# Performance work log

Measured on AMD Instinct MI355X. Metric: run time of the kernel, lower is better.

The kernel has to match this reference:

```python
import jax, jax.numpy as jnp
import numpy as np

EPS = 1e-5
K_NN = 5

def _bn(x, g, b, m, v):
    # BatchNorm1d in eval mode (running stats)
    return (x - m) * g / jnp.sqrt(v + EPS) + b

def _transf(x, w1, b1, g1, be1, m1, v1, w2, b2, g2, be2, m2, v2):
    h = jax.nn.relu(_bn(x @ w1.T + b1, g1, be1, m1, v1))
    return jax.nn.relu(_bn(h @ w2.T + b2, g2, be2, m2, v2))

def _cdist(x, y):
    # euclidean pairwise distance [Nq, Nk]
    d2 = jnp.sum(x * x, 1)[:, None] + jnp.sum(y * y, 1)[None, :] - 2.0 * (x @ y.T)
    return jnp.sqrt(jnp.clip(d2, 0.0))

def _to_pix(f):
    # [B,C,H,W] -> [B*H*W, C]
    B, C, H, W = f.shape
    return f.transpose(1, 0, 2, 3).reshape(C, -1).T

def _to_fmap(p, shape):
    B, C, H, W = shape
    return p.T.reshape(C, B, H, W).transpose(1, 0, 2, 3)

def _attend(dq, dk, aq, ak, vals, c1w, c1b, c2w, c2b):
    # full pairwise distance + hard kNN mask + softplus/softmax attention
    d = _cdist(dq, dk)                                  # [Nq, Nk]
    kth = -jax.lax.top_k(-d, K_NN)[0][:, K_NN - 1]       # K-th smallest per row
    # Conv1d(kernel_size = feat_dim) over length-feat_dim signal == dot product + bias
    att = (aq @ c1w + c1b)[:, None] + (ak @ c2w + c2b)[None, :]
    att = jax.nn.softplus(att) + jnp.where(d > kth[:, None], -1e9, 0.0)
    att = jax.nn.softmax(att, axis=1)
    return att @ vals

def _forward(inp_cont, inp_style, peers_cont, peers_style,
             w1c, b1c, g1c, be1c, m1c, v1c, w2c, b2c, g2c, be2c, m2c, v2c,
             c1cw, c1cb, c2cw, c2cb,
             w1s, b1s, g1s, be1s, m1s, v1s, w2s, b2s, g2s, be2s, m2s, v2s,
             c1sw, c1sb, c2sw, c2sb):
    ip = _to_pix(inp_cont)      # [N, C]
    pp = _to_pix(peers_cont)    # [N, C]
    ps = _to_pix(peers_style)   # [N, 2C]
    # recompose style: distance in content space, gather peer style
    aq = _transf(ip, w1c, b1c, g1c, be1c, m1c, v1c, w2c, b2c, g2c, be2c, m2c, v2c)
    ak = _transf(pp, w1c, b1c, g1c, be1c, m1c, v1c, w2c, b2c, g2c, be2c, m2c, v2c)
    out_sty = _attend(ip, pp, aq, ak, ps, c1cw, c1cb, c2cw, c2cb)   # [N, 2C]
    # recompose content: distance in (recomposed) style space, gather peer content
    sq = _transf(out_sty, w1s, b1s, g1s, be1s, m1s, v1s, w2s, b2s, g2s, be2s, m2s, v2s)
    sk = _transf(ps, w1s, b1s, g1s, be1s, m1s, v1s, w2s, b2s, g2s, be2s, m2s, v2s)
    out_cont = _attend(out_sty, ps, sq, sk, pp, c1sw, c1sb, c2sw, c2sb)  # [N, C]
    out_cont_f = _to_fmap(out_cont, inp_cont.shape)
    out_sty_f = _to_fmap(out_sty, inp_style.shape)
    return jnp.concatenate([out_cont_f, out_sty_f], axis=1)

def setup_inputs() -> dict:
    ks = jax.random.split(jax.random.key(0), 64)
    it = iter(range(64))
    rn = lambda sh, s=0.05: jax.random.normal(ks[next(it)], sh, jnp.float32) * s
    un = lambda sh: jax.random.uniform(ks[next(it)], sh, jnp.float32, 0.5, 1.5)
    C = 256; B = 1; H = W = 64
    return dict(
        inp_cont=rn((B, C, H, W), 1.0), inp_style=rn((B, 2 * C, H, W), 1.0),
        peers_cont=rn((B, C, H, W), 1.0), peers_style=rn((B, 2 * C, H, W), 1.0),
        w1c=rn((C // 2, C)), b1c=rn((C // 2,)), g1c=un((C // 2,)), be1c=rn((C // 2,)), m1c=rn((C // 2,)), v1c=un((C // 2,)),
        w2c=rn((C // 4, C // 2)), b2c=rn((C // 4,)), g2c=un((C // 4,)), be2c=rn((C // 4,)), m2c=rn((C // 4,)), v2c=un((C // 4,)),
        c1cw=rn((C // 4,)), c1cb=rn(()), c2cw=rn((C // 4,)), c2cb=rn(()),
        w1s=rn((C, 2 * C)), b1s=rn((C,)), g1s=un((C,)), be1s=rn((C,)), m1s=rn((C,)), v1s=un((C,)),
        w2s=rn((C // 2, C)), b2s=rn((C // 2,)), g2s=un((C // 2,)), be2s=rn((C // 2,)), m2s=rn((C // 2,)), v2s=un((C // 2,)),
        c1sw=rn((C // 2,)), c1sb=rn(()), c2sw=rn((C // 2,)), c2sb=rn(()),
    )

def reference(inp_cont, inp_style, peers_cont, peers_style,
              w1c, b1c, g1c, be1c, m1c, v1c, w2c, b2c, g2c, be2c, m2c, v2c,
              c1cw, c1cb, c2cw, c2cb,
              w1s, b1s, g1s, be1s, m1s, v1s, w2s, b2s, g2s, be2s, m2s, v2s,
              c1sw, c1sb, c2sw, c2sb):
    return _forward(inp_cont, inp_style, peers_cont, peers_style,
                    w1c, b1c, g1c, be1c, m1c, v1c, w2c, b2c, g2c, be2c, m2c, v2c,
                    c1cw, c1cb, c2cw, c2cb,
                    w1s, b1s, g1s, be1s, m1s, v1s, w2s, b2s, g2s, be2s, m2s, v2s,
                    c1sw, c1sb, c2sw, c2sb)
```

## Files before the change

kernel.cpp:

```cpp
#include <hip/hip_runtime.h>
#include <math.h>

#pragma clang fp contract(off)

#define NPIX 4096
#define BIGF 3.0e38f
#define SLOTS 8


__device__ __forceinline__ void ins5v(float v, float dl[5]) {
    if (v >= dl[4]) return;
    dl[4] = v;
#pragma unroll
    for (int u = 4; u > 0; --u)
        if (dl[u] < dl[u - 1]) { float t_ = dl[u]; dl[u] = dl[u - 1]; dl[u - 1] = t_; }
}

__device__ __forceinline__ float softplus_np(float x) {
    if (x > 0.f) {
        float ef = (float)exp((double)(-x));
        return x + (float)log1p((double)ef);
    } else if (x < 0.f) {
        float ef = (float)exp((double)x);
        return (float)log1p((double)ef);
    }
    return 0.69314718055994530942f;
}


__global__ __launch_bounds__(256) void gemm_bn_relu2_kernel(
    const float* __restrict__ W,
    const float* __restrict__ Xa, const float* __restrict__ Xb,
    const float* __restrict__ b, const float* __restrict__ g,
    const float* __restrict__ be, const float* __restrict__ m,
    const float* __restrict__ v,
    float* __restrict__ Ha, float* __restrict__ Hb, int M, int K) {
    const float* X = blockIdx.z ? Xb : Xa;
    float* H = blockIdx.z ? Hb : Ha;
    __shared__ float Ws[16][68];
    __shared__ float Xs[16][68];
    int t = threadIdx.x;
    int tx = t & 15, ty = t >> 4;
    int n0 = blockIdx.x * 64, m0 = blockIdx.y * 64;
    int wm = t >> 2, wk = (t & 3) * 4;
    int xk = t >> 4, xn = (t & 15) * 4;
    float acc[4][4] = {};
    for (int k0 = 0; k0 < K; k0 += 16) {
        float4 wv = *(const float4*)&W[(size_t)(m0 + wm) * K + k0 + wk];
        Ws[wk + 0][wm] = wv.x; Ws[wk + 1][wm] = wv.y;
        Ws[wk + 2][wm] = wv.z; Ws[wk + 3][wm] = wv.w;
        *(float4*)&Xs[xk][xn] = *(const float4*)&X[(size_t)(k0 + xk) * NPIX + n0 + xn];
        __syncthreads();
#pragma unroll
        for (int kk = 0; kk < 16; ++kk) {
            float4 a4 = *(float4*)&Ws[kk][ty * 4];
            float4 b4 = *(float4*)&Xs[kk][tx * 4];
            float ar[4] = {a4.x, a4.y, a4.z, a4.w};
            float br[4] = {b4.x, b4.y, b4.z, b4.w};
#pragma unroll
            for (int i = 0; i < 4; ++i)
#pragma unroll
                for (int j = 0; j < 4; ++j)
                    acc[i][j] = fmaf(ar[i], br[j], acc[i][j]);
        }
        __syncthreads();
    }
#pragma unroll
    for (int i = 0; i < 4; ++i) {
        int mrow = m0 + ty * 4 + i;
        float bb = b[mrow];
        float mm_ = m[mrow];
        float gg = g[mrow];
        float vv = v[mrow] + 1e-5f;
        float ss = (float)sqrt((double)vv);
        float bee = be[mrow];
        float o[4];
#pragma unroll
        for (int j = 0; j < 4; ++j) {
            float t0 = acc[i][j] + bb;
            t0 = t0 - mm_;
            t0 = t0 * gg;
            t0 = (float)((double)t0 / (double)ss);
            t0 = t0 + bee;
            o[j] = fmaxf(t0, 0.f);
        }
        *(float4*)&H[(size_t)mrow * NPIX + n0 + tx * 4] = *(float4*)&o[0];
    }
}


__global__ void dotk_np2_kernel(const float* __restrict__ Ha, const float* __restrict__ Hb,
                                const float* __restrict__ cwa, const float* __restrict__ cba,
                                const float* __restrict__ cwb, const float* __restrict__ cbb,
                                float* __restrict__ outa, float* __restrict__ outb, int C) {
    const float* H = blockIdx.z ? Hb : Ha;
    const float* cw = blockIdx.z ? cwb : cwa;
    const float* cb = blockIdx.z ? cbb : cba;
    float* out = blockIdx.z ? outb : outa;
    int p = blockIdx.x * 256 + threadIdx.x;
    float s = 0.f;
#pragma unroll 8
    for (int c = 0; c < C; ++c) s = fmaf(H[(size_t)c * NPIX + p], cw[c], s);
    out[p] = s + cb[0];
}


__global__ void skn_np2_kernel(const float* __restrict__ Ya, const float* __restrict__ Yb,
                               float* __restrict__ skna, float* __restrict__ sknb, int C) {
    const float* Y = blockIdx.z ? Yb : Ya;
    float* skn = blockIdx.z ? sknb : skna;
    int nb = C >> 7;
    int ppb = 256 / nb;
    int t = threadIdx.x;
    int pl = t % ppb;
    int b = t / ppb;
    int p = blockIdx.x * ppb + pl;
    __shared__ float sh[256];

    int c0 = b << 7;
    float r[8];
#pragma unroll
    for (int k = 0; k < 8; ++k) {
        float y = Y[(size_t)(c0 + k) * NPIX + p];
        r[k] = y * y;
    }
    for (int i = 8; i < 128; i += 8) {
#pragma unroll
        for (int k = 0; k < 8; ++k) {
            float y = Y[(size_t)(c0 + i + k) * NPIX + p];
            float q = y * y;
            r[k] = r[k] + q;
        }
    }
    sh[b * ppb + pl] = ((r[0] + r[1]) + (r[2] + r[3])) + ((r[4] + r[5]) + (r[6] + r[7]));
    __syncthreads();
    if (b == 0) {
        float s;
        if (nb == 2) s = sh[pl] + sh[ppb + pl];
        else s = (sh[pl] + sh[ppb + pl]) + (sh[2 * ppb + pl] + sh[3 * ppb + pl]);
        skn[p] = s;
    }
}


__global__ __launch_bounds__(256) void dist_np_kernel(
    const float* __restrict__ XT, const float* __restrict__ YT,
    const float* __restrict__ sknq, const float* __restrict__ sknk,
    float* __restrict__ D, int C, int qbase) {
    __shared__ float Xs[2][16][68];
    __shared__ float Ys[2][16][16][12];
    int t = threadIdx.x;
    int tx = t & 15, ty = t >> 4;
    int q0 = qbase + blockIdx.y * 64;
    int k0 = blockIdx.x * 128;
    float acc[4][8] = {};
    float4 xr = *(const float4*)&XT[(size_t)ty * NPIX + q0 + tx * 4];
    float4 yr0 = *(const float4*)&YT[(size_t)ty * NPIX + k0 + tx * 8];
    float4 yr1 = *(const float4*)&YT[(size_t)ty * NPIX + k0 + tx * 8 + 4];
    *(float4*)&Xs[0][ty][tx * 4] = xr;
    *(float4*)&Ys[0][ty][tx][0] = yr0;
    *(float4*)&Ys[0][ty][tx][4] = yr1;
    __syncthreads();
    int nt = C >> 4;
    for (int tt2 = 0; tt2 < nt; ++tt2) {
        int cur = tt2 & 1;
        if (tt2 + 1 < nt) {
            int cn = (tt2 + 1) << 4;
            xr = *(const float4*)&XT[(size_t)(cn + ty) * NPIX + q0 + tx * 4];
            yr0 = *(const float4*)&YT[(size_t)(cn + ty) * NPIX + k0 + tx * 8];
            yr1 = *(const float4*)&YT[(size_t)(cn + ty) * NPIX + k0 + tx * 8 + 4];
        }
#pragma unroll
        for (int kk = 0; kk < 16; ++kk) {
            float4 a4 = *(float4*)&Xs[cur][kk][ty * 4];
            float4 b40 = *(float4*)&Ys[cur][kk][tx][0];
            float4 b41 = *(float4*)&Ys[cur][kk][tx][4];
            float ar[4] = {a4.x, a4.y, a4.z, a4.w};
            float br[8] = {b40.x, b40.y, b40.z, b40.w, b41.x, b41.y, b41.z, b41.w};
#pragma unroll
            for (int i = 0; i < 4; ++i)
#pragma unroll
                for (int j = 0; j < 8; ++j)
                    acc[i][j] = fmaf(ar[i], br[j], acc[i][j]);
        }
        if (tt2 + 1 < nt) {
            *(float4*)&Xs[cur ^ 1][ty][tx * 4] = xr;
            *(float4*)&Ys[cur ^ 1][ty][tx][0] = yr0;
            *(float4*)&Ys[cur ^ 1][ty][tx][4] = yr1;
        }
        __syncthreads();
    }
    float sk8[8];
    *(float4*)&sk8[0] = *(const float4*)&sknk[k0 + tx * 8];
    *(float4*)&sk8[4] = *(const float4*)&sknk[k0 + tx * 8 + 4];
#pragma unroll
    for (int i = 0; i < 4; ++i) {
        float sq = sknq[q0 + ty * 4 + i];
        int lq = q0 - qbase + ty * 4 + i;
        float tmp[8];
#pragma unroll
        for (int j = 0; j < 8; ++j) {
            float A = sq + sk8[j];
            float B = 2.0f * acc[i][j];
            float d2 = A - B;
            float dc = fmaxf(d2, 0.f);
            tmp[j] = (float)sqrt((double)dc);
        }
        *(float4*)&D[(size_t)lq * NPIX + k0 + tx * 8] = *(float4*)&tmp[0];
        *(float4*)&D[(size_t)lq * NPIX + k0 + tx * 8 + 4] = *(float4*)&tmp[4];
    }
}


__global__ __launch_bounds__(256) void row_select_np_kernel(
    const float* __restrict__ D, const float* __restrict__ qs, const float* __restrict__ ks,
    int* __restrict__ isel, float* __restrict__ wsel, int qbase) {
    int p = qbase + blockIdx.x;
    const float* drow = D + (size_t)blockIdx.x * NPIX;
    int t = threadIdx.x;
    __shared__ float tops[256][5];
    __shared__ float l2[64][5];
    __shared__ float l3[16][5];
    __shared__ float kth_sh;
    __shared__ int cnt;
    __shared__ int slotj[16];
    __shared__ int n_sh;
    __shared__ float as_[16];
    __shared__ float evs[16];
    __shared__ float mx_sh, ssum_sh;

    if (t == 0) cnt = 0;
    float vcache[16];
    *(float4*)&vcache[0] = *(const float4*)&drow[t * 16];
    *(float4*)&vcache[4] = *(const float4*)&drow[t * 16 + 4];
    *(float4*)&vcache[8] = *(const float4*)&drow[t * 16 + 8];
    *(float4*)&vcache[12] = *(const float4*)&drow[t * 16 + 12];
    float dl[5] = {BIGF, BIGF, BIGF, BIGF, BIGF};
#pragma unroll
    for (int u = 0; u < 16; ++u) ins5v(vcache[u], dl);
#pragma unroll
    for (int u = 0; u < 5; ++u) tops[t][u] = dl[u];
    __syncthreads();
    if (t < 64) {
        float md[5] = {BIGF, BIGF, BIGF, BIGF, BIGF};
        for (int i = 0; i < 4; ++i)
            for (int u = 0; u < 5; ++u) ins5v(tops[t * 4 + i][u], md);
#pragma unroll
        for (int u = 0; u < 5; ++u) l2[t][u] = md[u];
    }
    __syncthreads();
    if (t < 16) {
        float md[5] = {BIGF, BIGF, BIGF, BIGF, BIGF};
        for (int i = 0; i < 4; ++i)
            for (int u = 0; u < 5; ++u) ins5v(l2[t * 4 + i][u], md);
#pragma unroll
        for (int u = 0; u < 5; ++u) l3[t][u] = md[u];
    }
    __syncthreads();
    if (t == 0) {
        float md[5] = {BIGF, BIGF, BIGF, BIGF, BIGF};
        for (int i = 0; i < 16; ++i)
            for (int u = 0; u < 5; ++u) ins5v(l3[i][u], md);
        kth_sh = md[4];
    }
    __syncthreads();
    float kth = kth_sh;
#pragma unroll
    for (int u = 0; u < 16; ++u) {
        if (vcache[u] <= kth) {
            int s = atomicAdd(&cnt, 1);
            if (s < 16) slotj[s] = t * 16 + u;
        }
    }
    __syncthreads();
    if (t == 0) {
        int n = cnt < 16 ? cnt : 16;
        for (int a = 1; a < n; ++a) {
            int key = slotj[a]; int b = a - 1;
            while (b >= 0 && slotj[b] > key) { slotj[b + 1] = slotj[b]; --b; }
            slotj[b + 1] = key;
        }
        n_sh = n;
    }
    __syncthreads();
    int n = n_sh;
    if (t < n) {
        float x = qs[p] + ks[slotj[t]];
        as_[t] = softplus_np(x);
    }
    __syncthreads();
    if (t == 0) {
        float mx = -BIGF;
        for (int s = 0; s < n; ++s) mx = fmaxf(mx, as_[s]);
        mx_sh = mx;
    }
    __syncthreads();
    if (t < n) evs[t] = (float)exp((double)(as_[t] - mx_sh));
    __syncthreads();
    if (t == 0) {
        float bs[32];
        for (int i = 0; i < 32; ++i) bs[i] = 0.f;
        int s2 = 0;
        while (s2 < n) {
            int b = slotj[s2] >> 7;
            float r[8] = {0.f, 0.f, 0.f, 0.f, 0.f, 0.f, 0.f, 0.f};
            while (s2 < n && (slotj[s2] >> 7) == b) {
                int res = slotj[s2] & 7;
                r[res] = r[res] + evs[s2];
                ++s2;
            }
            bs[b] = ((r[0] + r[1]) + (r[2] + r[3])) + ((r[4] + r[5]) + (r[6] + r[7]));
        }
        float t16[16], t8[8], t4[4], t2[2];
        for (int i = 0; i < 16; ++i) t16[i] = bs[2 * i] + bs[2 * i + 1];
        for (int i = 0; i < 8; ++i) t8[i] = t16[2 * i] + t16[2 * i + 1];
        for (int i = 0; i < 4; ++i) t4[i] = t8[2 * i] + t8[2 * i + 1];
        for (int i = 0; i < 2; ++i) t2[i] = t4[2 * i] + t4[2 * i + 1];
        ssum_sh = t2[0] + t2[1];
    }
    __syncthreads();
    if (t < SLOTS) {
        float w = (t < n) ? (float)((double)evs[t] / (double)ssum_sh) : 0.f;
        wsel[t * NPIX + p] = w;
        isel[t * NPIX + p] = (t < n) ? slotj[t] : 0;
    }
}


__global__ void gather_np_kernel(const float* __restrict__ V,
                                 const int* __restrict__ isel, const float* __restrict__ wsel,
                                 float* __restrict__ out, int CV) {
    int g = blockIdx.x * 256 + threadIdx.x;
    int p = g & (NPIX - 1);
    int c = g >> 12;
    if (c >= CV) return;
    const float* Vc = V + (size_t)c * NPIX;
    float s = 0.f;
#pragma unroll
    for (int tt = 0; tt < SLOTS; ++tt) {
        float w = wsel[tt * NPIX + p];
        int j = isel[tt * NPIX + p];
        s = fmaf(w, Vc[j], s);
    }
    out[(size_t)c * NPIX + p] = s;
}


extern "C" void kernel_launch(void* const* d_in, const int* in_sizes, int n_in,
                              void* d_out, int out_size, void* d_ws, size_t ws_size,
                              hipStream_t stream) {
    const float* ip = (const float*)d_in[0];
    const float* pp = (const float*)d_in[2];
    const float* ps = (const float*)d_in[3];
    const float* w1c = (const float*)d_in[4];
    const float* b1c = (const float*)d_in[5];
    const float* g1c = (const float*)d_in[6];
    const float* be1c = (const float*)d_in[7];
    const float* m1c = (const float*)d_in[8];
    const float* v1c = (const float*)d_in[9];
    const float* w2c = (const float*)d_in[10];
    const float* b2c = (const float*)d_in[11];
    const float* g2c = (const float*)d_in[12];
    const float* be2c = (const float*)d_in[13];
    const float* m2c = (const float*)d_in[14];
    const float* v2c = (const float*)d_in[15];
    const float* c1cw = (const float*)d_in[16];
    const float* c1cb = (const float*)d_in[17];
    const float* c2cw = (const float*)d_in[18];
    const float* c2cb = (const float*)d_in[19];
    const float* w1s = (const float*)d_in[20];
    const float* b1s = (const float*)d_in[21];
    const float* g1s = (const float*)d_in[22];
    const float* be1s = (const float*)d_in[23];
    const float* m1s = (const float*)d_in[24];
    const float* v1s = (const float*)d_in[25];
    const float* w2s = (const float*)d_in[26];
    const float* b2s = (const float*)d_in[27];
    const float* g2s = (const float*)d_in[28];
    const float* be2s = (const float*)d_in[29];
    const float* m2s = (const float*)d_in[30];
    const float* v2s = (const float*)d_in[31];
    const float* c1sw = (const float*)d_in[32];
    const float* c1sb = (const float*)d_in[33];
    const float* c2sw = (const float*)d_in[34];
    const float* c2sb = (const float*)d_in[35];

    float* out_cont = (float*)d_out;
    float* out_sty = (float*)d_out + 256 * NPIX;

    float* ws = (float*)d_ws;
    float* QS   = ws + 0;
    float* KS   = ws + 4096;
    float* SKNQ = ws + 8192;
    float* SKNK = ws + 12288;
    float* WSEL = ws + 16384;
    int*   ISEL = (int*)(ws + 49152);
    float* H1A  = ws + 81920;
    float* H1B  = ws + 1130496;
    float* H2A  = ws + 2179072;
    float* H2B  = ws + 2703360;
    float* D    = ws + 3227648;

    size_t base = 3227648;
    int chunk = 256;
    if (ws_size >= (base + (size_t)4096 * NPIX) * 4) chunk = 4096;
    else if (ws_size >= (base + (size_t)2048 * NPIX) * 4) chunk = 2048;
    else if (ws_size >= (base + (size_t)1024 * NPIX) * 4) chunk = 1024;
    else if (ws_size >= (base + (size_t)512 * NPIX) * 4) chunk = 512;
    int nch = NPIX / chunk;

    gemm_bn_relu2_kernel<<<dim3(64, 2, 2), 256, 0, stream>>>(
        w1c, ip, pp, b1c, g1c, be1c, m1c, v1c, H1A, H1B, 128, 256);
    gemm_bn_relu2_kernel<<<dim3(64, 1, 2), 256, 0, stream>>>(
        w2c, H1A, H1B, b2c, g2c, be2c, m2c, v2c, H2A, H2B, 64, 128);
    dotk_np2_kernel<<<dim3(16, 1, 2), 256, 0, stream>>>(
        H2A, H2B, c1cw, c1cb, c2cw, c2cb, QS, KS, 64);
    skn_np2_kernel<<<dim3(32, 1, 2), 256, 0, stream>>>(ip, pp, SKNQ, SKNK, 256);
    for (int ch = 0; ch < nch; ++ch) {
        dist_np_kernel<<<dim3(32, chunk / 64), 256, 0, stream>>>(ip, pp, SKNQ, SKNK, D, 256, ch * chunk);
        row_select_np_kernel<<<chunk, 256, 0, stream>>>(D, QS, KS, ISEL, WSEL, ch * chunk);
    }
    gather_np_kernel<<<(512 * NPIX) / 256, 256, 0, stream>>>(ps, ISEL, WSEL, out_sty, 512);

    gemm_bn_relu2_kernel<<<dim3(64, 4, 2), 256, 0, stream>>>(
        w1s, out_sty, ps, b1s, g1s, be1s, m1s, v1s, H1A, H1B, 256, 512);
    gemm_bn_relu2_kernel<<<dim3(64, 2, 2), 256, 0, stream>>>(
        w2s, H1A, H1B, b2s, g2s, be2s, m2s, v2s, H2A, H2B, 128, 256);
    dotk_np2_kernel<<<dim3(16, 1, 2), 256, 0, stream>>>(
        H2A, H2B, c1sw, c1sb, c2sw, c2sb, QS, KS, 128);
    skn_np2_kernel<<<dim3(64, 1, 2), 256, 0, stream>>>(out_sty, ps, SKNQ, SKNK, 512);
    for (int ch = 0; ch < nch; ++ch) {
        dist_np_kernel<<<dim3(32, chunk / 64), 256, 0, stream>>>(out_sty, ps, SKNQ, SKNK, D, 512, ch * chunk);
        row_select_np_kernel<<<chunk, 256, 0, stream>>>(D, QS, KS, ISEL, WSEL, ch * chunk);
    }
    gather_np_kernel<<<(256 * NPIX) / 256, 256, 0, stream>>>(pp, ISEL, WSEL, out_cont, 256);
}
```

Before: 561.9 us.

## Merge dot-product and squared-norm kernels; single-buffer LDS in distance GEMM

The per-pixel attention dot-product and squared-norm kernels are merged into one launch that picks its task from blockIdx.y, removing one launch per stage. Separately, the distance GEMM goes from double-buffered to single-buffered shared-memory tiles with a register prefetch, halving LDS use per block, which may allow more blocks per CU. The cost is an extra barrier per tile, so shared-memory stores no longer overlap the FMA loop, plus some idle blocks in the merged launch that exit early.

```diff
diff --git a/kernel.cpp b/kernel.cpp
--- a/kernel.cpp
+++ b/kernel.cpp
@@ -89,56 +89,59 @@
 }
 
 
-__global__ void dotk_np2_kernel(const float* __restrict__ Ha, const float* __restrict__ Hb,
-                                const float* __restrict__ cwa, const float* __restrict__ cba,
-                                const float* __restrict__ cwb, const float* __restrict__ cbb,
-                                float* __restrict__ outa, float* __restrict__ outb, int C) {
-    const float* H = blockIdx.z ? Hb : Ha;
-    const float* cw = blockIdx.z ? cwb : cwa;
-    const float* cb = blockIdx.z ? cbb : cba;
-    float* out = blockIdx.z ? outb : outa;
-    int p = blockIdx.x * 256 + threadIdx.x;
-    float s = 0.f;
+__global__ void util_np_kernel(
+    const float* __restrict__ H2A, const float* __restrict__ H2B,
+    const float* __restrict__ cwa, const float* __restrict__ cba,
+    const float* __restrict__ cwb, const float* __restrict__ cbb,
+    float* __restrict__ QS, float* __restrict__ KS, int CH,
+    const float* __restrict__ Yq, const float* __restrict__ Yk,
+    float* __restrict__ SKNQ, float* __restrict__ SKNK, int CY) {
+    int task = blockIdx.y;
+    int t = threadIdx.x;
+    if (task < 2) {
+        if (blockIdx.x >= 16) return;
+        const float* H = task ? H2B : H2A;
+        const float* cw = task ? cwb : cwa;
+        const float* cb = task ? cbb : cba;
+        float* out = task ? KS : QS;
+        int p = blockIdx.x * 256 + t;
+        float s = 0.f;
 #pragma unroll 8
-    for (int c = 0; c < C; ++c) s = fmaf(H[(size_t)c * NPIX + p], cw[c], s);
-    out[p] = s + cb[0];
-}
-
-
-__global__ void skn_np2_kernel(const float* __restrict__ Ya, const float* __restrict__ Yb,
-                               float* __restrict__ skna, float* __restrict__ sknb, int C) {
-    const float* Y = blockIdx.z ? Yb : Ya;
-    float* skn = blockIdx.z ? sknb : skna;
-    int nb = C >> 7;
-    int ppb = 256 / nb;
-    int t = threadIdx.x;
-    int pl = t % ppb;
-    int b = t / ppb;
-    int p = blockIdx.x * ppb + pl;
-    __shared__ float sh[256];
-
-    int c0 = b << 7;
-    float r[8];
-#pragma unroll
-    for (int k = 0; k < 8; ++k) {
-        float y = Y[(size_t)(c0 + k) * NPIX + p];
-        r[k] = y * y;
-    }
-    for (int i = 8; i < 128; i += 8) {
+        for (int c = 0; c < CH; ++c) s = fmaf(H[(size_t)c * NPIX + p], cw[c], s);
+        out[p] = s + cb[0];
+    } else {
+        const float* Y = (task == 2) ? Yq : Yk;
+        float* skn = (task == 2) ? SKNQ : SKNK;
+        int nb = CY >> 7;
+        int ppb = 256 / nb;
+        if (blockIdx.x * ppb >= NPIX) return;
+        int pl = t % ppb;
+        int b = t / ppb;
+        int p = blockIdx.x * ppb + pl;
+        __shared__ float sh[256];
+        int c0 = b << 7;
+        float r[8];
 #pragma unroll
         for (int k = 0; k < 8; ++k) {
-            float y = Y[(size_t)(c0 + i + k) * NPIX + p];
-            float q = y * y;
-            r[k] = r[k] + q;
-        }
-    }
-    sh[b * ppb + pl] = ((r[0] + r[1]) + (r[2] + r[3])) + ((r[4] + r[5]) + (r[6] + r[7]));
-    __syncthreads();
-    if (b == 0) {
-        float s;
-        if (nb == 2) s = sh[pl] + sh[ppb + pl];
-        else s = (sh[pl] + sh[ppb + pl]) + (sh[2 * ppb + pl] + sh[3 * ppb + pl]);
-        skn[p] = s;
+            float y = Y[(size_t)(c0 + k) * NPIX + p];
+            r[k] = y * y;
+        }
+        for (int i = 8; i < 128; i += 8) {
+#pragma unroll
+            for (int k = 0; k < 8; ++k) {
+                float y = Y[(size_t)(c0 + i + k) * NPIX + p];
+                float q = y * y;
+                r[k] = r[k] + q;
+            }
+        }
+        sh[b * ppb + pl] = ((r[0] + r[1]) + (r[2] + r[3])) + ((r[4] + r[5]) + (r[6] + r[7]));
+        __syncthreads();
+        if (b == 0) {
+            float s;
+            if (nb == 2) s = sh[pl] + sh[ppb + pl];
+            else s = (sh[pl] + sh[ppb + pl]) + (sh[2 * ppb + pl] + sh[3 * ppb + pl]);
+            skn[p] = s;
+        }
     }
 }
 
@@ -147,8 +150,8 @@
     const float* __restrict__ XT, const float* __restrict__ YT,
     const float* __restrict__ sknq, const float* __restrict__ sknk,
     float* __restrict__ D, int C, int qbase) {
-    __shared__ float Xs[2][16][68];
-    __shared__ float Ys[2][16][16][12];
+    __shared__ float Xs[16][68];
+    __shared__ float Ys[16][16][12];
     int t = threadIdx.x;
     int tx = t & 15, ty = t >> 4;
     int q0 = qbase + blockIdx.y * 64;
@@ -157,24 +160,21 @@
     float4 xr = *(const float4*)&XT[(size_t)ty * NPIX + q0 + tx * 4];
     float4 yr0 = *(const float4*)&YT[(size_t)ty * NPIX + k0 + tx * 8];
     float4 yr1 = *(const float4*)&YT[(size_t)ty * NPIX + k0 + tx * 8 + 4];
-    *(float4*)&Xs[0][ty][tx * 4] = xr;
-    *(float4*)&Ys[0][ty][tx][0] = yr0;
-    *(float4*)&Ys[0][ty][tx][4] = yr1;
-    __syncthreads();
-    int nt = C >> 4;
-    for (int tt2 = 0; tt2 < nt; ++tt2) {
-        int cur = tt2 & 1;
-        if (tt2 + 1 < nt) {
-            int cn = (tt2 + 1) << 4;
-            xr = *(const float4*)&XT[(size_t)(cn + ty) * NPIX + q0 + tx * 4];
-            yr0 = *(const float4*)&YT[(size_t)(cn + ty) * NPIX + k0 + tx * 8];
-            yr1 = *(const float4*)&YT[(size_t)(cn + ty) * NPIX + k0 + tx * 8 + 4];
+    for (int c0 = 0; c0 < C; c0 += 16) {
+        *(float4*)&Xs[ty][tx * 4] = xr;
+        *(float4*)&Ys[ty][tx][0] = yr0;
+        *(float4*)&Ys[ty][tx][4] = yr1;
+        __syncthreads();
+        if (c0 + 16 < C) {
+            xr = *(const float4*)&XT[(size_t)(c0 + 16 + ty) * NPIX + q0 + tx * 4];
+            yr0 = *(const float4*)&YT[(size_t)(c0 + 16 + ty) * NPIX + k0 + tx * 8];
+            yr1 = *(const float4*)&YT[(size_t)(c0 + 16 + ty) * NPIX + k0 + tx * 8 + 4];
         }
 #pragma unroll
         for (int kk = 0; kk < 16; ++kk) {
-            float4 a4 = *(float4*)&Xs[cur][kk][ty * 4];
-            float4 b40 = *(float4*)&Ys[cur][kk][tx][0];
-            float4 b41 = *(float4*)&Ys[cur][kk][tx][4];
+            float4 a4 = *(float4*)&Xs[kk][ty * 4];
+            float4 b40 = *(float4*)&Ys[kk][tx][0];
+            float4 b41 = *(float4*)&Ys[kk][tx][4];
             float ar[4] = {a4.x, a4.y, a4.z, a4.w};
             float br[8] = {b40.x, b40.y, b40.z, b40.w, b41.x, b41.y, b41.z, b41.w};
 #pragma unroll
@@ -182,11 +182,6 @@
 #pragma unroll
                 for (int j = 0; j < 8; ++j)
                     acc[i][j] = fmaf(ar[i], br[j], acc[i][j]);
-        }
-        if (tt2 + 1 < nt) {
-            *(float4*)&Xs[cur ^ 1][ty][tx * 4] = xr;
-            *(float4*)&Ys[cur ^ 1][ty][tx][0] = yr0;
-            *(float4*)&Ys[cur ^ 1][ty][tx][4] = yr1;
         }
         __syncthreads();
     }
@@ -413,9 +408,9 @@
         w1c, ip, pp, b1c, g1c, be1c, m1c, v1c, H1A, H1B, 128, 256);
     gemm_bn_relu2_kernel<<<dim3(64, 1, 2), 256, 0, stream>>>(
         w2c, H1A, H1B, b2c, g2c, be2c, m2c, v2c, H2A, H2B, 64, 128);
-    dotk_np2_kernel<<<dim3(16, 1, 2), 256, 0, stream>>>(
-        H2A, H2B, c1cw, c1cb, c2cw, c2cb, QS, KS, 64);
-    skn_np2_kernel<<<dim3(32, 1, 2), 256, 0, stream>>>(ip, pp, SKNQ, SKNK, 256);
+    util_np_kernel<<<dim3(64, 4), 256, 0, stream>>>(
+        H2A, H2B, c1cw, c1cb, c2cw, c2cb, QS, KS, 64,
+        ip, pp, SKNQ, SKNK, 256);
     for (int ch = 0; ch < nch; ++ch) {
         dist_np_kernel<<<dim3(32, chunk / 64), 256, 0, stream>>>(ip, pp, SKNQ, SKNK, D, 256, ch * chunk);
         row_select_np_kernel<<<chunk, 256, 0, stream>>>(D, QS, KS, ISEL, WSEL, ch * chunk);
@@ -426,9 +421,9 @@
         w1s, out_sty, ps, b1s, g1s, be1s, m1s, v1s, H1A, H1B, 256, 512);
     gemm_bn_relu2_kernel<<<dim3(64, 2, 2), 256, 0, stream>>>(
         w2s, H1A, H1B, b2s, g2s, be2s, m2s, v2s, H2A, H2B, 128, 256);
-    dotk_np2_kernel<<<dim3(16, 1, 2), 256, 0, stream>>>(
-        H2A, H2B, c1sw, c1sb, c2sw, c2sb, QS, KS, 128);
-    skn_np2_kernel<<<dim3(64, 1, 2), 256, 0, stream>>>(out_sty, ps, SKNQ, SKNK, 512);
+    util_np_kernel<<<dim3(64, 4), 256, 0, stream>>>(
+        H2A, H2B, c1sw, c1sb, c2sw, c2sb, QS, KS, 128,
+        out_sty, ps, SKNQ, SKNK, 512);
     for (int ch = 0; ch < nch; ++ch) {
         dist_np_kernel<<<dim3(32, chunk / 64), 256, 0, stream>>>(out_sty, ps, SKNQ, SKNK, D, 512, ch * chunk);
         row_select_np_kernel<<<chunk, 256, 0, stream>>>(D, QS, KS, ISEL, WSEL, ch * chunk);
```

Measured after the change: 535.2 us. 1.05x faster.
